# Kernel tuning notes

Hardware: AMD Instinct MI355X
Metric: run time of the kernel (lower is better)

Reference implementation:

```python
import jax, jax.numpy as jnp
import numpy as np

B, NP, K = 8, 512, 64   # graphs, points per graph, knn neighbors
N = B * NP              # total nodes
EPS = 1e-5


def knn_edges(pos):
    """knn_graph(pos, k=K, batch, loop=True): edges (src=j neighbor, dst=i)."""
    p = pos.reshape(B, NP, 3)
    d2 = jnp.sum((p[:, :, None, :] - p[:, None, :, :]) ** 2, axis=-1)  # [B,NP,NP]
    _, idx = jax.lax.top_k(-d2, K)  # [B,NP,K] nearest (self included, d2=0)
    off = (jnp.arange(B, dtype=jnp.int32) * NP)[:, None, None]
    src = (idx.astype(jnp.int32) + off).reshape(-1)
    dst = jnp.broadcast_to(jnp.arange(NP, dtype=jnp.int32)[None, :, None] + off,
                           (B, NP, K)).reshape(-1)
    return src, dst


def graph_norm(x, batch, w, b, ms):
    """PyG GraphNorm: per-graph mean/std with learnable mean scale."""
    cnt = jax.ops.segment_sum(jnp.ones((x.shape[0], 1), x.dtype), batch, B)
    mean = jax.ops.segment_sum(x, batch, B) / cnt
    out = x - mean[batch] * ms
    var = jax.ops.segment_sum(out * out, batch, B) / cnt
    return w * out / jnp.sqrt(var + EPS)[batch] + b


def pointnet_layer(h, pos, src, dst, w1, b1, w2, b2):
    """message = MLP(concat(h_j, pos_j - pos_i)); aggregate = scatter-max over dst."""
    m = jnp.concatenate([h[src], pos[src] - pos[dst]], axis=-1)  # [E, Cin+3]
    m = jax.nn.relu(m @ w1 + b1) @ w2 + b2                        # [E, Cout]
    return jax.ops.segment_max(m, dst, N)


def _forward(batch, pos,
             gn1_w, gn1_b, gn1_ms, gn2_w, gn2_b, gn2_ms, gn3_w, gn3_b, gn3_ms,
             gn4_w, gn4_b, gn4_ms, gn5_w, gn5_b, gn5_ms, gn6_w, gn6_b, gn6_ms,
             c1_w1, c1_b1, c1_w2, c1_b2, c2_w1, c2_b1, c2_w2, c2_b2,
             c3_w1, c3_b1, c3_w2, c3_b2, c4_w1, c4_b1, c4_w2, c4_b2,
             c5_w1, c5_b1, c5_w2, c5_b2, cls_w, cls_b):
    src, dst = knn_edges(pos)
    h = graph_norm(pos, batch, gn1_w, gn1_b, gn1_ms)
    h = pointnet_layer(h, pos, src, dst, c1_w1, c1_b1, c1_w2, c1_b2)
    h = jax.nn.relu(graph_norm(h, batch, gn2_w, gn2_b, gn2_ms))
    h = pointnet_layer(h, pos, src, dst, c2_w1, c2_b1, c2_w2, c2_b2)
    h = jax.nn.relu(graph_norm(h, batch, gn3_w, gn3_b, gn3_ms))
    h = pointnet_layer(h, pos, src, dst, c3_w1, c3_b1, c3_w2, c3_b2)
    h = jax.nn.relu(graph_norm(h, batch, gn4_w, gn4_b, gn4_ms))
    h = pointnet_layer(h, pos, src, dst, c4_w1, c4_b1, c4_w2, c4_b2)
    h = jax.nn.relu(graph_norm(h, batch, gn5_w, gn5_b, gn5_ms))
    h = pointnet_layer(h, pos, src, dst, c5_w1, c5_b1, c5_w2, c5_b2)
    h = jax.nn.relu(graph_norm(h, batch, gn6_w, gn6_b, gn6_ms))
    return h @ cls_w + cls_b  # [N, 14]


def setup_inputs() -> dict:
    key = jax.random.key(0)
    ks = iter(jax.random.split(key, 40))
    inp = {}
    inp["pos"] = jax.random.normal(next(ks), (N, 3), jnp.float32)
    inp["batch"] = jnp.repeat(jnp.arange(B, dtype=jnp.int32), NP)
    for i, c in enumerate([3, 64, 128, 256, 512, 512], 1):
        inp[f"gn{i}_w"] = jnp.ones((c,), jnp.float32)
        inp[f"gn{i}_b"] = jnp.zeros((c,), jnp.float32)
        inp[f"gn{i}_ms"] = jnp.ones((c,), jnp.float32)
    for i, (ci, co) in enumerate([(3, 64), (64, 128), (128, 256), (256, 512), (512, 512)], 1):
        fin = ci + 3
        inp[f"c{i}_w1"] = jax.random.normal(next(ks), (fin, co), jnp.float32) / np.sqrt(fin).astype(np.float32)
        inp[f"c{i}_b1"] = jnp.zeros((co,), jnp.float32)
        inp[f"c{i}_w2"] = jax.random.normal(next(ks), (co, co), jnp.float32) / np.sqrt(co).astype(np.float32)
        inp[f"c{i}_b2"] = jnp.zeros((co,), jnp.float32)
    inp["cls_w"] = jax.random.normal(next(ks), (512, 14), jnp.float32) / np.float32(np.sqrt(512))
    inp["cls_b"] = jnp.zeros((14,), jnp.float32)
    return inp


def reference(pos, batch,
              gn1_w, gn1_b, gn1_ms, gn2_w, gn2_b, gn2_ms, gn3_w, gn3_b, gn3_ms,
              gn4_w, gn4_b, gn4_ms, gn5_w, gn5_b, gn5_ms, gn6_w, gn6_b, gn6_ms,
              c1_w1, c1_b1, c1_w2, c1_b2, c2_w1, c2_b1, c2_w2, c2_b2,
              c3_w1, c3_b1, c3_w2, c3_b2, c4_w1, c4_b1, c4_w2, c4_b2,
              c5_w1, c5_b1, c5_w2, c5_b2, cls_w, cls_b):
    return _forward(batch, pos,
                    gn1_w, gn1_b, gn1_ms, gn2_w, gn2_b, gn2_ms, gn3_w, gn3_b, gn3_ms,
                    gn4_w, gn4_b, gn4_ms, gn5_w, gn5_b, gn5_ms, gn6_w, gn6_b, gn6_ms,
                    c1_w1, c1_b1, c1_w2, c1_b2, c2_w1, c2_b1, c2_w2, c2_b2,
                    c3_w1, c3_b1, c3_w2, c3_b2, c4_w1, c4_b1, c4_w2, c4_b2,
                    c5_w1, c5_b1, c5_w2, c5_b2, cls_w, cls_b)
```

## Files before the change

### kernel.cpp

```cpp
#include <hip/hip_runtime.h>
#include <stdint.h>

#define N_NODES 4096
#define NGRAPH 8
#define NPTS 512
#define KNN 64
#define EPSN 1e-5f

typedef _Float16 f16x8 __attribute__((ext_vector_type(8)));
typedef float f32x4 __attribute__((ext_vector_type(4)));
typedef unsigned long long u64;

__device__ __forceinline__ unsigned short f2h(float f) {
    _Float16 h = (_Float16)f;
    union { _Float16 h; unsigned short u; } cv; cv.h = h;
    return cv.u;
}

__device__ __forceinline__ void w2cv(const float* __restrict__ src, unsigned short* __restrict__ dst,
                                     int off, int lg2c) {
    int C = 1 << lg2c;
    int k = off >> lg2c, n = off & (C - 1);
    int d = ((n >> 4) * (C / 32) + (k >> 5)) * 512 + ((k >> 3) & 3) * 128 + (n & 15) * 8 + (k & 7);
    dst[d] = f2h(src[off]);
}

__global__ __launch_bounds__(64) void setup_kernel(const float* __restrict__ pos, int* __restrict__ knn_out,
                                                   const float* __restrict__ wa, const float* __restrict__ wb,
                                                   const float* __restrict__ wc, const float* __restrict__ wd,
                                                   const float* __restrict__ we,
                                                   unsigned short* __restrict__ oa, unsigned short* __restrict__ ob,
                                                   unsigned short* __restrict__ oc, unsigned short* __restrict__ od,
                                                   unsigned short* __restrict__ oe,
                                                   float* __restrict__ statz,
                                                   const float* __restrict__ ms1, const float* __restrict__ gw1,
                                                   float* __restrict__ Aa, float* __restrict__ Sa) {
#pragma clang fp contract(off)
    __shared__ float px[NPTS], py[NPTS], pz[NPTS];
    __shared__ u64 keys[NPTS];
    int bid = blockIdx.x;
    int tid = threadIdx.x;
    int gidx = bid * 64 + tid;
    for (int idx = gidx; idx < 40960; idx += 262144) statz[idx] = 0.f;
    for (int idx = gidx; idx < 610304; idx += 262144) {
        if (idx < 4096)        w2cv(wa, oa, idx, 6);
        else if (idx < 20480)  w2cv(wb, ob, idx - 4096, 7);
        else if (idx < 86016)  w2cv(wc, oc, idx - 20480, 8);
        else if (idx < 348160) w2cv(wd, od, idx - 86016, 9);
        else                   w2cv(we, oe, idx - 348160, 9);
    }
    if (bid < 24) {
        int g = bid / 3, ch = bid - g * 3;
        float s1 = 0.f, s2 = 0.f;
        for (int n = tid; n < NPTS; n += 64) {
            float v = pos[(g * NPTS + n) * 3 + ch];
            s1 += v; s2 += v * v;
        }
        #pragma unroll
        for (int off = 32; off; off >>= 1) { s1 += __shfl_xor(s1, off); s2 += __shfl_xor(s2, off); }
        if (tid == 0) {
            float mean = s1 * (1.f / NPTS);
            float av = mean * ms1[ch];
            float var = s2 * (1.f / NPTS) - 2.f * av * mean + av * av;
            Aa[g * 3 + ch] = av;
            Sa[g * 3 + ch] = gw1[ch] / sqrtf(var + EPSN);
        }
    }
    int b = bid >> 9;
    int il = bid & (NPTS - 1);
    for (int n = tid; n < NPTS; n += 64) {
        int base = (b * NPTS + n) * 3;
        px[n] = pos[base]; py[n] = pos[base + 1]; pz[n] = pos[base + 2];
    }
    __syncthreads();
    float xi = px[il], yi = py[il], zi = pz[il];
    for (int n = tid; n < NPTS; n += 64) {
        float dx = px[n] - xi, dy = py[n] - yi, dz = pz[n] - zi;
        float d2 = dx * dx;
        d2 = d2 + dy * dy;
        d2 = d2 + dz * dz;
        keys[n] = (((u64)__float_as_uint(d2)) << 32) | (unsigned)n;
    }
    __syncthreads();
    for (int k2 = 2; k2 <= NPTS; k2 <<= 1) {
        for (int j = k2 >> 1; j > 0; j >>= 1) {
            #pragma unroll 4
            for (int p = 0; p < 4; ++p) {
                int pid = tid + p * 64;
                int t = ((pid & ~(j - 1)) << 1) | (pid & (j - 1));
                int ixj = t | j;
                u64 a = keys[t], c = keys[ixj];
                bool up = ((t & k2) == 0);
                if ((a > c) == up) { keys[t] = c; keys[ixj] = a; }
            }
            __syncthreads();
        }
    }
    int j0 = (int)(keys[tid] & 0xffffffffu);
    knn_out[(size_t)(b * NPTS + il) * KNN + tid] = b * NPTS + j0;
}

template<int CIN, int C, int RELU, int RAW>
__global__ __launch_bounds__(C) void node_kernel(const float* __restrict__ y, const float* __restrict__ pos,
                                                 const float* __restrict__ p1, const float* __restrict__ p2,
                                                 const float* __restrict__ ms, const float* __restrict__ gw,
                                                 const float* __restrict__ bnp,
                                                 const float* __restrict__ w1, const float* __restrict__ b1,
                                                 float* __restrict__ U, float* __restrict__ P) {
    constexpr int ROWS = 16;
    constexpr int KC = 64;
    constexpr int LDH = KC + 4;
    __shared__ float hs[ROWS][LDH];
    __shared__ float As_[CIN > 0 ? CIN : 1], Ss_[CIN > 0 ? CIN : 1];
    const int c = threadIdx.x;
    const int n0 = blockIdx.x * ROWS;
    const int b = n0 >> 9;
    if (RAW) {
        for (int ch = c; ch < CIN; ch += C) {
            float s1 = p1[b * CIN + ch], s2 = p2[b * CIN + ch];
            float mean = s1 * (1.f / NPTS);
            float a = mean * ms[ch];
            float var = s2 * (1.f / NPTS) - 2.f * a * mean + a * a;
            As_[ch] = a;
            Ss_[ch] = gw[ch] / sqrtf(var + EPSN);
        }
    }
    float acc[ROWS];
    #pragma unroll
    for (int r = 0; r < ROWS; ++r) acc[r] = 0.f;
    constexpr int NCHUNK = (CIN + KC - 1) / KC;
    #pragma unroll 1
    for (int s = 0; s < NCHUNK; ++s) {
        const int k0 = s * KC;
        const int kc = (CIN - k0 < KC) ? (CIN - k0) : KC;
        __syncthreads();
        for (int idx = c; idx < ROWS * kc; idx += C) {
            int r = idx / kc, k = idx - r * kc;
            int ch = k0 + k;
            float a = RAW ? As_[ch] : p1[b * CIN + ch];
            float sf = RAW ? Ss_[ch] : p2[b * CIN + ch];
            float v = (y[(size_t)(n0 + r) * CIN + ch] - a) * sf + bnp[ch];
            if (RELU) v = fmaxf(v, 0.f);
            hs[r][k] = v;
        }
        __syncthreads();
        int k = 0;
        for (; k + 4 <= kc; k += 4) {
            float w0 = w1[(size_t)(k0 + k) * C + c];
            float w1v = w1[(size_t)(k0 + k + 1) * C + c];
            float w2v = w1[(size_t)(k0 + k + 2) * C + c];
            float w3v = w1[(size_t)(k0 + k + 3) * C + c];
            #pragma unroll
            for (int r = 0; r < ROWS; ++r) {
                f32x4 hv = *(const f32x4*)&hs[r][k];
                acc[r] = fmaf(hv[0], w0, acc[r]);
                acc[r] = fmaf(hv[1], w1v, acc[r]);
                acc[r] = fmaf(hv[2], w2v, acc[r]);
                acc[r] = fmaf(hv[3], w3v, acc[r]);
            }
        }
        for (; k < kc; ++k) {
            float wv = w1[(size_t)(k0 + k) * C + c];
            #pragma unroll
            for (int r = 0; r < ROWS; ++r)
                acc[r] = fmaf(hs[r][k], wv, acc[r]);
        }
    }
    float pacc[ROWS];
    #pragma unroll
    for (int r = 0; r < ROWS; ++r) pacc[r] = 0.f;
    #pragma unroll
    for (int e = 0; e < 3; ++e) {
        float wv = w1[(size_t)(CIN + e) * C + c];
        #pragma unroll
        for (int r = 0; r < ROWS; ++r)
            pacc[r] = fmaf(pos[(n0 + r) * 3 + e], wv, pacc[r]);
    }
    float bv = b1[c];
    #pragma unroll
    for (int r = 0; r < ROWS; ++r) {
        U[(size_t)(n0 + r) * C + c] = acc[r] + pacc[r] + bv;
        P[(size_t)(n0 + r) * C + c] = pacc[r];
    }
}

template<int C, int W>
__global__ __launch_bounds__(W * 64, 4) void edge_kernel(const float* __restrict__ U, const float* __restrict__ P,
                                                         const int* __restrict__ knn, const unsigned short* __restrict__ w2t,
                                                         const float* __restrict__ b2, float* __restrict__ Y,
                                                         float* __restrict__ sum1, float* __restrict__ sum2) {
    constexpr int NCT = C / (W * 16);
    constexpr int S32 = C / 32;
    constexpr int NCHUNK = C / 8;
    __shared__ unsigned short Th[64 * C];
    __shared__ int jn[64];
    __shared__ float Pr[C];
    const int bid = blockIdx.x;
    const int i = ((bid & 7) << 9) | (bid >> 3);
    const int tid = threadIdx.x;
    const int wave = tid >> 6, lane = tid & 63, m = lane & 15, quad = lane >> 4;
    const int cw = wave * (NCT * 16);
    if (tid < 64) jn[tid] = knn[(size_t)i * KNN + tid];
    for (int idx = tid; idx < C; idx += W * 64) Pr[idx] = P[(size_t)i * C + idx];
    __syncthreads();
    #pragma unroll 2
    for (int idx = tid; idx < 64 * NCHUNK; idx += W * 64) {
        int row = idx / NCHUNK, ch = idx - row * NCHUNK;
        const float* up = U + (size_t)jn[row] * C + ch * 8;
        f32x4 va = *(const f32x4*)up;
        f32x4 vb = *(const f32x4*)(up + 4);
        f32x4 pa = *(const f32x4*)&Pr[ch * 8];
        f32x4 pb = *(const f32x4*)&Pr[ch * 8 + 4];
        uint4 pk;
        pk.x = (unsigned)f2h(fmaxf(va[0] - pa[0], 0.f)) | ((unsigned)f2h(fmaxf(va[1] - pa[1], 0.f)) << 16);
        pk.y = (unsigned)f2h(fmaxf(va[2] - pa[2], 0.f)) | ((unsigned)f2h(fmaxf(va[3] - pa[3], 0.f)) << 16);
        pk.z = (unsigned)f2h(fmaxf(vb[0] - pb[0], 0.f)) | ((unsigned)f2h(fmaxf(vb[1] - pb[1], 0.f)) << 16);
        pk.w = (unsigned)f2h(fmaxf(vb[2] - pb[2], 0.f)) | ((unsigned)f2h(fmaxf(vb[3] - pb[3], 0.f)) << 16);
        int sc = (ch & ~7) | ((ch ^ row) & 7);
        *(uint4*)&Th[row * C + sc * 8] = pk;
    }
    __syncthreads();
    f32x4 acc[4][NCT];
    f32x4 zero = {0.f, 0.f, 0.f, 0.f};
    #pragma unroll
    for (int rt = 0; rt < 4; ++rt)
        #pragma unroll
        for (int ct = 0; ct < NCT; ++ct)
            acc[rt][ct] = zero;
    #pragma unroll 2
    for (int s = 0; s < S32; ++s) {
        f16x8 a[4];
        #pragma unroll
        for (int rt = 0; rt < 4; ++rt) {
            int row = rt * 16 + m;
            int chunk = s * 4 + quad;
            int sc = (chunk & ~7) | ((chunk ^ row) & 7);
            a[rt] = *(const f16x8*)&Th[row * C + sc * 8];
        }
        #pragma unroll
        for (int ct = 0; ct < NCT; ++ct) {
            const f16x8 bb = *(const f16x8*)(w2t +
                (size_t)(((cw >> 4) + ct) * S32 + s) * 512 + quad * 128 + m * 8);
            #pragma unroll
            for (int rt = 0; rt < 4; ++rt)
                acc[rt][ct] = __builtin_amdgcn_mfma_f32_16x16x32_f16(a[rt], bb, acc[rt][ct], 0, 0, 0);
        }
    }
    const int gb = i >> 9;
    #pragma unroll
    for (int ct = 0; ct < NCT; ++ct) {
        float vmax = -3.4e38f;
        #pragma unroll
        for (int rt = 0; rt < 4; ++rt) {
            vmax = fmaxf(vmax, acc[rt][ct][0]);
            vmax = fmaxf(vmax, acc[rt][ct][1]);
            vmax = fmaxf(vmax, acc[rt][ct][2]);
            vmax = fmaxf(vmax, acc[rt][ct][3]);
        }
        vmax = fmaxf(vmax, __shfl_xor(vmax, 16));
        vmax = fmaxf(vmax, __shfl_xor(vmax, 32));
        if (quad == 0) {
            int col = cw + ct * 16 + m;
            float val = vmax + b2[col];
            Y[(size_t)i * C + col] = val;
            atomicAdd(&sum1[gb * C + col], val);
            atomicAdd(&sum2[gb * C + col], val * val);
        }
    }
}

__global__ __launch_bounds__(256) void cls_kernel(const float* __restrict__ y, const float* __restrict__ sum1,
                                                  const float* __restrict__ sum2, const float* __restrict__ ms,
                                                  const float* __restrict__ gw, const float* __restrict__ gnb,
                                                  const float* __restrict__ w, const float* __restrict__ bias,
                                                  float* __restrict__ out) {
    __shared__ float wl[512 * 14];
    __shared__ _Float16 hn[16][520];
    __shared__ float As[512], Ss[512];
    int tid = threadIdx.x;
    int n0 = blockIdx.x * 16;
    int b = n0 >> 9;
    for (int ch = tid; ch < 512; ch += 256) {
        float s1 = sum1[b * 512 + ch], s2 = sum2[b * 512 + ch];
        float mean = s1 * (1.f / NPTS);
        float a = mean * ms[ch];
        float var = s2 * (1.f / NPTS) - 2.f * a * mean + a * a;
        As[ch] = a;
        Ss[ch] = gw[ch] / sqrtf(var + EPSN);
    }
    for (int idx = tid; idx < 512 * 14; idx += 256) wl[idx] = w[idx];
    __syncthreads();
    for (int idx = tid; idx < 16 * 512; idx += 256) {
        int r = idx >> 9, k = idx & 511;
        float v = (y[(size_t)(n0 + r) * 512 + k] - As[k]) * Ss[k] + gnb[k];
        hn[r][k] = (_Float16)fmaxf(v, 0.f);
    }
    __syncthreads();
    if (tid < 224) {
        int nl = tid / 14, c = tid - nl * 14;
        float acc = bias[c];
        for (int k = 0; k < 512; ++k)
            acc += (float)hn[nl][k] * wl[k * 14 + c];
        out[(size_t)(n0 + nl) * 14 + c] = acc;
    }
}

extern "C" void kernel_launch(void* const* d_in, const int* in_sizes, int n_in,
                              void* d_out, int out_size, void* d_ws, size_t ws_size,
                              hipStream_t stream) {
    const float* pos = (const float*)d_in[0];
    const float* gnw[6]; const float* gnb[6]; const float* gnms[6];
    for (int i = 0; i < 6; ++i) {
        gnw[i]  = (const float*)d_in[2 + 3 * i];
        gnb[i]  = (const float*)d_in[3 + 3 * i];
        gnms[i] = (const float*)d_in[4 + 3 * i];
    }
    const float* cw1[5]; const float* cb1[5]; const float* cw2[5]; const float* cb2[5];
    for (int i = 0; i < 5; ++i) {
        cw1[i] = (const float*)d_in[20 + 4 * i];
        cb1[i] = (const float*)d_in[21 + 4 * i];
        cw2[i] = (const float*)d_in[22 + 4 * i];
        cb2[i] = (const float*)d_in[23 + 4 * i];
    }
    const float* clsw = (const float*)d_in[40];
    const float* clsb = (const float*)d_in[41];
    float* out = (float*)d_out;

    char* ws = (char*)d_ws;
    int* knn             = (int*)(ws + 0);
    float* U             = (float*)(ws + 1048576);
    float* P             = (float*)(ws + 9437184);
    float* y             = (float*)(ws + 26214400);
    float* Aa            = (float*)(ws + 34603008);
    float* Sa            = (float*)(ws + 34619392);
    unsigned short* w2t0 = (unsigned short*)(ws + 34635776);
    unsigned short* w2t1 = (unsigned short*)(ws + 34643968);
    unsigned short* w2t2 = (unsigned short*)(ws + 34676736);
    unsigned short* w2t3 = (unsigned short*)(ws + 34807808);
    unsigned short* w2t4 = (unsigned short*)(ws + 35332096);
    float* acc           = (float*)(ws + 35856384);
    float* s1l[5]; float* s2l[5];
    for (int l = 0; l < 5; ++l) { s1l[l] = acc + l * 8192; s2l[l] = s1l[l] + 4096; }

    setup_kernel<<<N_NODES, 64, 0, stream>>>(pos, knn, cw2[0], cw2[1], cw2[2], cw2[3], cw2[4],
                                             w2t0, w2t1, w2t2, w2t3, w2t4, acc,
                                             gnms[0], gnw[0], Aa, Sa);

    node_kernel<3, 64, 0, 0><<<N_NODES / 16, 64, 0, stream>>>(pos, pos, Aa, Sa, gnms[0], gnw[0], gnb[0], cw1[0], cb1[0], U, P);
    edge_kernel<64, 4><<<N_NODES, 256, 0, stream>>>(U, P, knn, w2t0, cb2[0], y, s1l[0], s2l[0]);

    node_kernel<64, 128, 1, 1><<<N_NODES / 16, 128, 0, stream>>>(y, pos, s1l[0], s2l[0], gnms[1], gnw[1], gnb[1], cw1[1], cb1[1], U, P);
    edge_kernel<128, 8><<<N_NODES, 512, 0, stream>>>(U, P, knn, w2t1, cb2[1], y, s1l[1], s2l[1]);

    node_kernel<128, 256, 1, 1><<<N_NODES / 16, 256, 0, stream>>>(y, pos, s1l[1], s2l[1], gnms[2], gnw[2], gnb[2], cw1[2], cb1[2], U, P);
    edge_kernel<256, 8><<<N_NODES, 512, 0, stream>>>(U, P, knn, w2t2, cb2[2], y, s1l[2], s2l[2]);

    node_kernel<256, 512, 1, 1><<<N_NODES / 16, 512, 0, stream>>>(y, pos, s1l[2], s2l[2], gnms[3], gnw[3], gnb[3], cw1[3], cb1[3], U, P);
    edge_kernel<512, 8><<<N_NODES, 512, 0, stream>>>(U, P, knn, w2t3, cb2[3], y, s1l[3], s2l[3]);

    node_kernel<512, 512, 1, 1><<<N_NODES / 16, 512, 0, stream>>>(y, pos, s1l[3], s2l[3], gnms[4], gnw[4], gnb[4], cw1[4], cb1[4], U, P);
    edge_kernel<512, 8><<<N_NODES, 512, 0, stream>>>(U, P, knn, w2t4, cb2[4], y, s1l[4], s2l[4]);

    cls_kernel<<<N_NODES / 16, 256, 0, stream>>>(y, s1l[4], s2l[4], gnms[5], gnw[5], gnb[5], clsw, clsb, out);
}
```

Measured before the change: 713.3 us.

## Process two destination nodes per edge-kernel block to reuse W2 fragments

Each edge block now handles two destination nodes, 128 neighbor rows instead of 64, so every W2 fragment loaded from global memory feeds eight MFMA row tiles instead of four. The grid is halved and the per-node P vectors are held in registers instead of shared memory. Shared memory per block doubles (128 KB of staging for C=512) and the accumulator count doubles, which lowers occupancy and adds register pressure. Launch bounds drop to 2 blocks per CU to match.

```diff
diff --git a/kernel.cpp b/kernel.cpp
--- a/kernel.cpp
+++ b/kernel.cpp
@@ -185,32 +185,40 @@
 }
 
 template<int C, int W>
-__global__ __launch_bounds__(W * 64, 4) void edge_kernel(const float* __restrict__ U, const float* __restrict__ P,
+__global__ __launch_bounds__(W * 64, 2) void edge_kernel(const float* __restrict__ U, const float* __restrict__ P,
                                                          const int* __restrict__ knn, const unsigned short* __restrict__ w2t,
                                                          const float* __restrict__ b2, float* __restrict__ Y,
                                                          float* __restrict__ sum1, float* __restrict__ sum2) {
     constexpr int NCT = C / (W * 16);
     constexpr int S32 = C / 32;
     constexpr int NCHUNK = C / 8;
-    __shared__ unsigned short Th[64 * C];
-    __shared__ int jn[64];
-    __shared__ float Pr[C];
+    constexpr int STEP = (W * 64) / NCHUNK;
+    constexpr int T = 128 / STEP;
+    __shared__ unsigned short Th[128 * C];
+    __shared__ int jn[128];
     const int bid = blockIdx.x;
-    const int i = ((bid & 7) << 9) | (bid >> 3);
+    const int g = bid & 7;
+    const int n0 = (g << 9) | ((bid >> 3) << 1);
     const int tid = threadIdx.x;
     const int wave = tid >> 6, lane = tid & 63, m = lane & 15, quad = lane >> 4;
     const int cw = wave * (NCT * 16);
-    if (tid < 64) jn[tid] = knn[(size_t)i * KNN + tid];
-    for (int idx = tid; idx < C; idx += W * 64) Pr[idx] = P[(size_t)i * C + idx];
-    __syncthreads();
-    #pragma unroll 2
-    for (int idx = tid; idx < 64 * NCHUNK; idx += W * 64) {
-        int row = idx / NCHUNK, ch = idx - row * NCHUNK;
+    if (tid < 128) jn[tid] = knn[(size_t)(n0 + (tid >> 6)) * KNN + (tid & 63)];
+    const int ch = tid & (NCHUNK - 1);
+    const int rbase = tid >> (31 - __builtin_clz(NCHUNK));
+    const float* p0 = P + (size_t)n0 * C + ch * 8;
+    f32x4 pa0 = *(const f32x4*)p0;
+    f32x4 pb0 = *(const f32x4*)(p0 + 4);
+    f32x4 pa1 = *(const f32x4*)(p0 + C);
+    f32x4 pb1 = *(const f32x4*)(p0 + C + 4);
+    __syncthreads();
+    #pragma unroll 4
+    for (int t = 0; t < T; ++t) {
+        int row = rbase + t * STEP;
         const float* up = U + (size_t)jn[row] * C + ch * 8;
         f32x4 va = *(const f32x4*)up;
         f32x4 vb = *(const f32x4*)(up + 4);
-        f32x4 pa = *(const f32x4*)&Pr[ch * 8];
-        f32x4 pb = *(const f32x4*)&Pr[ch * 8 + 4];
+        f32x4 pa = (row & 64) ? pa1 : pa0;
+        f32x4 pb = (row & 64) ? pb1 : pb0;
         uint4 pk;
         pk.x = (unsigned)f2h(fmaxf(va[0] - pa[0], 0.f)) | ((unsigned)f2h(fmaxf(va[1] - pa[1], 0.f)) << 16);
         pk.y = (unsigned)f2h(fmaxf(va[2] - pa[2], 0.f)) | ((unsigned)f2h(fmaxf(va[3] - pa[3], 0.f)) << 16);
@@ -220,18 +228,18 @@
         *(uint4*)&Th[row * C + sc * 8] = pk;
     }
     __syncthreads();
-    f32x4 acc[4][NCT];
+    f32x4 acc[8][NCT];
     f32x4 zero = {0.f, 0.f, 0.f, 0.f};
     #pragma unroll
-    for (int rt = 0; rt < 4; ++rt)
+    for (int rt = 0; rt < 8; ++rt)
         #pragma unroll
         for (int ct = 0; ct < NCT; ++ct)
             acc[rt][ct] = zero;
-    #pragma unroll 2
+    #pragma unroll 1
     for (int s = 0; s < S32; ++s) {
-        f16x8 a[4];
-        #pragma unroll
-        for (int rt = 0; rt < 4; ++rt) {
+        f16x8 a[8];
+        #pragma unroll
+        for (int rt = 0; rt < 8; ++rt) {
             int row = rt * 16 + m;
             int chunk = s * 4 + quad;
             int sc = (chunk & ~7) | ((chunk ^ row) & 7);
@@ -242,29 +250,31 @@
             const f16x8 bb = *(const f16x8*)(w2t +
                 (size_t)(((cw >> 4) + ct) * S32 + s) * 512 + quad * 128 + m * 8);
             #pragma unroll
-            for (int rt = 0; rt < 4; ++rt)
+            for (int rt = 0; rt < 8; ++rt)
                 acc[rt][ct] = __builtin_amdgcn_mfma_f32_16x16x32_f16(a[rt], bb, acc[rt][ct], 0, 0, 0);
         }
     }
-    const int gb = i >> 9;
-    #pragma unroll
-    for (int ct = 0; ct < NCT; ++ct) {
-        float vmax = -3.4e38f;
-        #pragma unroll
-        for (int rt = 0; rt < 4; ++rt) {
-            vmax = fmaxf(vmax, acc[rt][ct][0]);
-            vmax = fmaxf(vmax, acc[rt][ct][1]);
-            vmax = fmaxf(vmax, acc[rt][ct][2]);
-            vmax = fmaxf(vmax, acc[rt][ct][3]);
-        }
-        vmax = fmaxf(vmax, __shfl_xor(vmax, 16));
-        vmax = fmaxf(vmax, __shfl_xor(vmax, 32));
-        if (quad == 0) {
-            int col = cw + ct * 16 + m;
-            float val = vmax + b2[col];
-            Y[(size_t)i * C + col] = val;
-            atomicAdd(&sum1[gb * C + col], val);
-            atomicAdd(&sum2[gb * C + col], val * val);
+    #pragma unroll
+    for (int h = 0; h < 2; ++h) {
+        #pragma unroll
+        for (int ct = 0; ct < NCT; ++ct) {
+            float vmax = -3.4e38f;
+            #pragma unroll
+            for (int rt = h * 4; rt < h * 4 + 4; ++rt) {
+                vmax = fmaxf(vmax, acc[rt][ct][0]);
+                vmax = fmaxf(vmax, acc[rt][ct][1]);
+                vmax = fmaxf(vmax, acc[rt][ct][2]);
+                vmax = fmaxf(vmax, acc[rt][ct][3]);
+            }
+            vmax = fmaxf(vmax, __shfl_xor(vmax, 16));
+            vmax = fmaxf(vmax, __shfl_xor(vmax, 32));
+            if (quad == 0) {
+                int col = cw + ct * 16 + m;
+                float val = vmax + b2[col];
+                Y[(size_t)(n0 + h) * C + col] = val;
+                atomicAdd(&sum1[g * C + col], val);
+                atomicAdd(&sum2[g * C + col], val * val);
+            }
         }
     }
 }
@@ -347,19 +357,19 @@
                                              gnms[0], gnw[0], Aa, Sa);
 
     node_kernel<3, 64, 0, 0><<<N_NODES / 16, 64, 0, stream>>>(pos, pos, Aa, Sa, gnms[0], gnw[0], gnb[0], cw1[0], cb1[0], U, P);
-    edge_kernel<64, 4><<<N_NODES, 256, 0, stream>>>(U, P, knn, w2t0, cb2[0], y, s1l[0], s2l[0]);
+    edge_kernel<64, 4><<<N_NODES / 2, 256, 0, stream>>>(U, P, knn, w2t0, cb2[0], y, s1l[0], s2l[0]);
 
     node_kernel<64, 128, 1, 1><<<N_NODES / 16, 128, 0, stream>>>(y, pos, s1l[0], s2l[0], gnms[1], gnw[1], gnb[1], cw1[1], cb1[1], U, P);
-    edge_kernel<128, 8><<<N_NODES, 512, 0, stream>>>(U, P, knn, w2t1, cb2[1], y, s1l[1], s2l[1]);
+    edge_kernel<128, 8><<<N_NODES / 2, 512, 0, stream>>>(U, P, knn, w2t1, cb2[1], y, s1l[1], s2l[1]);
 
     node_kernel<128, 256, 1, 1><<<N_NODES / 16, 256, 0, stream>>>(y, pos, s1l[1], s2l[1], gnms[2], gnw[2], gnb[2], cw1[2], cb1[2], U, P);
-    edge_kernel<256, 8><<<N_NODES, 512, 0, stream>>>(U, P, knn, w2t2, cb2[2], y, s1l[2], s2l[2]);
+    edge_kernel<256, 8><<<N_NODES / 2, 512, 0, stream>>>(U, P, knn, w2t2, cb2[2], y, s1l[2], s2l[2]);
 
     node_kernel<256, 512, 1, 1><<<N_NODES / 16, 512, 0, stream>>>(y, pos, s1l[2], s2l[2], gnms[3], gnw[3], gnb[3], cw1[3], cb1[3], U, P);
-    edge_kernel<512, 8><<<N_NODES, 512, 0, stream>>>(U, P, knn, w2t3, cb2[3], y, s1l[3], s2l[3]);
+    edge_kernel<512, 8><<<N_NODES / 2, 512, 0, stream>>>(U, P, knn, w2t3, cb2[3], y, s1l[3], s2l[3]);
 
     node_kernel<512, 512, 1, 1><<<N_NODES / 16, 512, 0, stream>>>(y, pos, s1l[3], s2l[3], gnms[4], gnw[4], gnb[4], cw1[4], cb1[4], U, P);
-    edge_kernel<512, 8><<<N_NODES, 512, 0, stream>>>(U, P, knn, w2t4, cb2[4], y, s1l[4], s2l[4]);
+    edge_kernel<512, 8><<<N_NODES / 2, 512, 0, stream>>>(U, P, knn, w2t4, cb2[4], y, s1l[4], s2l[4]);
 
     cls_kernel<<<N_NODES / 16, 256, 0, stream>>>(y, s1l[4], s2l[4], gnms[5], gnw[5], gnb[5], clsw, clsb, out);
 }
```

Result: slower. 746.0 us (+4.6%).

## Process two nodes per block in wide-channel edge kernels with double-buffered LDS tiles

Applied to the files above, without the earlier changes.

Adds an edge2_kernel that handles two destination nodes (128 edges) per block, so each W2 fragment loaded from global memory feeds eight MFMA row tiles instead of four. The gathered U rows minus P are converted to fp16 into a swizzled, double-buffered LDS tile, with the next 64-channel chunk prefetched while the current one is multiplied. It is used for the 256- and 512-channel layers. The intent is to halve W2 traffic per edge and overlap gather with compute, at the cost of more accumulator registers (launch_bounds 512,2) and half as many blocks.

```diff
diff --git a/kernel.cpp b/kernel.cpp
--- a/kernel.cpp
+++ b/kernel.cpp
@@ -269,6 +269,124 @@
     }
 }
 
+__device__ __forceinline__ uint4 pack8(f32x4 va, f32x4 vb, f32x4 pa, f32x4 pb) {
+    uint4 pk;
+    pk.x = (unsigned)f2h(fmaxf(va[0] - pa[0], 0.f)) | ((unsigned)f2h(fmaxf(va[1] - pa[1], 0.f)) << 16);
+    pk.y = (unsigned)f2h(fmaxf(va[2] - pa[2], 0.f)) | ((unsigned)f2h(fmaxf(va[3] - pa[3], 0.f)) << 16);
+    pk.z = (unsigned)f2h(fmaxf(vb[0] - pb[0], 0.f)) | ((unsigned)f2h(fmaxf(vb[1] - pb[1], 0.f)) << 16);
+    pk.w = (unsigned)f2h(fmaxf(vb[2] - pb[2], 0.f)) | ((unsigned)f2h(fmaxf(vb[3] - pb[3], 0.f)) << 16);
+    return pk;
+}
+
+template<int C>
+__global__ __launch_bounds__(512, 2) void edge2_kernel(const float* __restrict__ U, const float* __restrict__ P,
+                                                       const int* __restrict__ knn, const unsigned short* __restrict__ w2t,
+                                                       const float* __restrict__ b2, float* __restrict__ Y,
+                                                       float* __restrict__ sum1, float* __restrict__ sum2) {
+    constexpr int NCT = C / 128;
+    constexpr int S32 = C / 32;
+    constexpr int NCH = C / 64;
+    __shared__ unsigned short Th[2][128 * 64];
+    __shared__ float Pr[2 * C];
+    __shared__ int jn[128];
+    const int bid = blockIdx.x;
+    const int g = bid & 7;
+    const int n0 = (g << 9) | ((bid >> 3) << 1);
+    const int tid = threadIdx.x;
+    const int lane = tid & 63, wave = tid >> 6, m = lane & 15, quad = lane >> 4;
+    const int cw = wave * (NCT * 16);
+    if (tid < 128) jn[tid] = knn[(size_t)(n0 + (tid >> 6)) * KNN + (tid & 63)];
+    for (int idx = tid; idx < 2 * C; idx += 512) Pr[idx] = P[(size_t)n0 * C + idx];
+    const int srow = tid >> 2;
+    const int sgrp = tid & 3;
+    const int wbase = srow * 64;
+    const int sw0 = (((2 * sgrp) ^ (srow & 7)) << 3);
+    const int sw1 = (((2 * sgrp + 1) ^ (srow & 7)) << 3);
+    const float* pbase = Pr + (srow >> 6) * C + sgrp * 16;
+    __syncthreads();
+    const float* ubase = U + (size_t)jn[srow] * C + sgrp * 16;
+    f32x4 uf[4];
+    #pragma unroll
+    for (int q = 0; q < 4; ++q) uf[q] = *(const f32x4*)(ubase + q * 4);
+    {
+        f32x4 p0 = *(const f32x4*)(pbase);
+        f32x4 p1 = *(const f32x4*)(pbase + 4);
+        f32x4 p2 = *(const f32x4*)(pbase + 8);
+        f32x4 p3 = *(const f32x4*)(pbase + 12);
+        *(uint4*)&Th[0][wbase + sw0] = pack8(uf[0], uf[1], p0, p1);
+        *(uint4*)&Th[0][wbase + sw1] = pack8(uf[2], uf[3], p2, p3);
+    }
+    __syncthreads();
+    f32x4 acc[8][NCT];
+    f32x4 zero = {0.f, 0.f, 0.f, 0.f};
+    #pragma unroll
+    for (int rt = 0; rt < 8; ++rt)
+        #pragma unroll
+        for (int ct = 0; ct < NCT; ++ct)
+            acc[rt][ct] = zero;
+    #pragma unroll 1
+    for (int c = 0; c < NCH; ++c) {
+        const bool more = (c + 1 < NCH);
+        if (more) {
+            const float* up = ubase + (c + 1) * 64;
+            #pragma unroll
+            for (int q = 0; q < 4; ++q) uf[q] = *(const f32x4*)(up + q * 4);
+        }
+        const unsigned short* tb = Th[c & 1];
+        #pragma unroll
+        for (int ks = 0; ks < 2; ++ks) {
+            f16x8 a[8];
+            #pragma unroll
+            for (int rt = 0; rt < 8; ++rt) {
+                int row = rt * 16 + m;
+                a[rt] = *(const f16x8*)&tb[row * 64 + (((ks * 4 + quad) ^ (row & 7)) << 3)];
+            }
+            #pragma unroll
+            for (int ct = 0; ct < NCT; ++ct) {
+                const f16x8 bb = *(const f16x8*)(w2t +
+                    (size_t)((((cw >> 4) + ct) * S32 + (c * 2 + ks)) * 512 + quad * 128 + m * 8));
+                #pragma unroll
+                for (int rt = 0; rt < 8; ++rt)
+                    acc[rt][ct] = __builtin_amdgcn_mfma_f32_16x16x32_f16(a[rt], bb, acc[rt][ct], 0, 0, 0);
+            }
+        }
+        if (more) {
+            const float* pb = pbase + (c + 1) * 64;
+            f32x4 p0 = *(const f32x4*)(pb);
+            f32x4 p1 = *(const f32x4*)(pb + 4);
+            f32x4 p2 = *(const f32x4*)(pb + 8);
+            f32x4 p3 = *(const f32x4*)(pb + 12);
+            unsigned short* tn = Th[(c + 1) & 1];
+            *(uint4*)&tn[wbase + sw0] = pack8(uf[0], uf[1], p0, p1);
+            *(uint4*)&tn[wbase + sw1] = pack8(uf[2], uf[3], p2, p3);
+        }
+        __syncthreads();
+    }
+    #pragma unroll
+    for (int h = 0; h < 2; ++h) {
+        #pragma unroll
+        for (int ct = 0; ct < NCT; ++ct) {
+            float vmax = -3.4e38f;
+            #pragma unroll
+            for (int rt = h * 4; rt < h * 4 + 4; ++rt) {
+                vmax = fmaxf(vmax, acc[rt][ct][0]);
+                vmax = fmaxf(vmax, acc[rt][ct][1]);
+                vmax = fmaxf(vmax, acc[rt][ct][2]);
+                vmax = fmaxf(vmax, acc[rt][ct][3]);
+            }
+            vmax = fmaxf(vmax, __shfl_xor(vmax, 16));
+            vmax = fmaxf(vmax, __shfl_xor(vmax, 32));
+            if (quad == 0) {
+                int col = cw + ct * 16 + m;
+                float val = vmax + b2[col];
+                Y[(size_t)(n0 + h) * C + col] = val;
+                atomicAdd(&sum1[g * C + col], val);
+                atomicAdd(&sum2[g * C + col], val * val);
+            }
+        }
+    }
+}
+
 __global__ __launch_bounds__(256) void cls_kernel(const float* __restrict__ y, const float* __restrict__ sum1,
                                                   const float* __restrict__ sum2, const float* __restrict__ ms,
                                                   const float* __restrict__ gw, const float* __restrict__ gnb,
@@ -353,13 +471,13 @@
     edge_kernel<128, 8><<<N_NODES, 512, 0, stream>>>(U, P, knn, w2t1, cb2[1], y, s1l[1], s2l[1]);
 
     node_kernel<128, 256, 1, 1><<<N_NODES / 16, 256, 0, stream>>>(y, pos, s1l[1], s2l[1], gnms[2], gnw[2], gnb[2], cw1[2], cb1[2], U, P);
-    edge_kernel<256, 8><<<N_NODES, 512, 0, stream>>>(U, P, knn, w2t2, cb2[2], y, s1l[2], s2l[2]);
+    edge2_kernel<256><<<N_NODES / 2, 512, 0, stream>>>(U, P, knn, w2t2, cb2[2], y, s1l[2], s2l[2]);
 
     node_kernel<256, 512, 1, 1><<<N_NODES / 16, 512, 0, stream>>>(y, pos, s1l[2], s2l[2], gnms[3], gnw[3], gnb[3], cw1[3], cb1[3], U, P);
-    edge_kernel<512, 8><<<N_NODES, 512, 0, stream>>>(U, P, knn, w2t3, cb2[3], y, s1l[3], s2l[3]);
+    edge2_kernel<512><<<N_NODES / 2, 512, 0, stream>>>(U, P, knn, w2t3, cb2[3], y, s1l[3], s2l[3]);
 
     node_kernel<512, 512, 1, 1><<<N_NODES / 16, 512, 0, stream>>>(y, pos, s1l[3], s2l[3], gnms[4], gnw[4], gnb[4], cw1[4], cb1[4], U, P);
-    edge_kernel<512, 8><<<N_NODES, 512, 0, stream>>>(U, P, knn, w2t4, cb2[4], y, s1l[4], s2l[4]);
+    edge2_kernel<512><<<N_NODES / 2, 512, 0, stream>>>(U, P, knn, w2t4, cb2[4], y, s1l[4], s2l[4]);
 
     cls_kernel<<<N_NODES / 16, 256, 0, stream>>>(y, s1l[4], s2l[4], gnms[5], gnw[5], gnb[5], clsw, clsb, out);
 }
```

Result: slower. 794.4 us (+11.4%).
